# Performance work log

Hardware: AMD Instinct MI355X
Metric: run time of the kernel (lower is better)

Reference implementation:

```python
import jax, jax.numpy as jnp
import numpy as np
import math

D = 1024      # d_model
H = 4096      # expert hidden
E = 8         # num_experts
K = 2         # top_k
CAP_FACTOR = 1.25
B, S = 4, 2048
T = B * S
CAP = int(math.ceil(CAP_FACTOR * T * K / E))  # 2560


def setup_inputs() -> dict:
    key = jax.random.key(0)
    ks = jax.random.split(key, 6)
    x  = jax.random.normal(ks[0], (B, S, D), dtype=jnp.float32)
    Wr = jax.random.normal(ks[1], (D, E), dtype=jnp.float32) * (1.0 / np.sqrt(D))
    W1 = jax.random.normal(ks[2], (E, D, H), dtype=jnp.float32) * (1.0 / np.sqrt(D))
    b1 = jnp.zeros((E, H), dtype=jnp.float32)
    W2 = jax.random.normal(ks[3], (E, H, D), dtype=jnp.float32) * (1.0 / np.sqrt(H))
    b2 = jnp.zeros((E, D), dtype=jnp.float32)
    return {"x": x, "Wr": Wr, "W1": W1, "b1": b1, "W2": W2, "b2": b2}


def reference(x, Wr, W1, b1, W2, b2):
    x_flat = x.reshape(T, D)

    # ---- Router: top-k softmax gating (temp = 1.0), renormalized weights ----
    logits = jnp.einsum('td,de->te', x_flat, Wr)
    probs = jax.nn.softmax(logits, axis=-1)
    topk_w, topk_idx = jax.lax.top_k(probs, K)            # [T,K]
    topk_w = topk_w / jnp.sum(topk_w, axis=-1, keepdims=True)

    # ---- Vectorized capacity-based dispatch ----
    e = topk_idx.reshape(-1)                               # [T*K] expert id per pair
    onehot = jax.nn.one_hot(e, E, dtype=jnp.int32)         # [T*K, E]
    pos_all = jnp.cumsum(onehot, axis=0) - 1               # slot within expert
    pos = jnp.take_along_axis(pos_all, e[:, None], axis=1)[:, 0]
    keep = pos < CAP
    # dropped pairs go to a dummy slot E*CAP (sliced off / zero-padded)
    dest = jnp.where(keep, e * CAP + pos, E * CAP)         # [T*K]

    x_pairs = jnp.repeat(x_flat, K, axis=0)                # [T*K, D]
    buf = jnp.zeros((E * CAP + 1, D), dtype=x.dtype).at[dest].set(x_pairs)
    expert_in = buf[:E * CAP].reshape(E, CAP, D)

    # ---- Grouped expert MLP (GELU) ----
    h = jax.nn.gelu(jnp.einsum('ecd,edh->ech', expert_in, W1) + b1[:, None, :])
    expert_out = jnp.einsum('ech,ehd->ecd', h, W2) + b2[:, None, :]

    # ---- Combine: gather back and weight; dropped tokens get zeros ----
    out_pad = jnp.concatenate(
        [expert_out.reshape(E * CAP, D), jnp.zeros((1, D), dtype=x.dtype)], axis=0)
    y_pairs = out_pad[dest] * topk_w.reshape(-1)[:, None]  # [T*K, D]
    y_flat = y_pairs.reshape(T, K, D).sum(axis=1)
    return y_flat.reshape(B, S, D)
```

## Files before the change

### kernel.cpp

```cpp
#include <hip/hip_runtime.h>
#include <stdint.h>

#define D_MODEL 1024
#define H_DIM   4096
#define NE      8
#define NCAP    2560
#define NTOK    8192
#define NPAIR   (NTOK * 2)

typedef __attribute__((ext_vector_type(8))) __bf16 bf16x8;
typedef __attribute__((ext_vector_type(4))) float  f32x4;
typedef __attribute__((ext_vector_type(8))) unsigned short ushort8;

__device__ __forceinline__ unsigned short f2bf(float f) {
  union { float f; unsigned u; } v; v.f = f;
  unsigned r = v.u + 0x7fffu + ((v.u >> 16) & 1u);
  return (unsigned short)(r >> 16);
}
__device__ __forceinline__ float bf2f(unsigned short s) {
  union { unsigned u; float f; } v; v.u = ((unsigned)s) << 16;
  return v.f;
}
__device__ __forceinline__ float gelu_tanh(float x) {
  float u = 0.7978845608028654f * (x + 0.044715f * x * x * x);
  float e = __expf(2.0f * u);
  float th = 1.0f - 2.0f / (e + 1.0f);
  return 0.5f * x * (1.0f + th);
}
__device__ __forceinline__ void load_lds16(const void* g, void* l) {
  __builtin_amdgcn_global_load_lds(
      (const __attribute__((address_space(1))) unsigned int*)g,
      (__attribute__((address_space(3))) unsigned int*)l, 16, 0, 0);
}

__global__ __launch_bounds__(256) void router_kernel(
    const float* __restrict__ x, const float* __restrict__ Wr,
    int* __restrict__ pair_e, float* __restrict__ pair_w) {
  int lane = threadIdx.x & 63;
  int t = blockIdx.x * 4 + (threadIdx.x >> 6);
  float acc[NE];
#pragma unroll
  for (int e = 0; e < NE; ++e) acc[e] = 0.0f;
  const float* xr = x + (size_t)t * D_MODEL;
  for (int d = lane; d < D_MODEL; d += 64) {
    float xv = xr[d];
#pragma unroll
    for (int e = 0; e < NE; ++e) acc[e] = fmaf(xv, Wr[d * NE + e], acc[e]);
  }
#pragma unroll
  for (int off = 32; off > 0; off >>= 1) {
#pragma unroll
    for (int e = 0; e < NE; ++e) acc[e] += __shfl_down(acc[e], off, 64);
  }
  if (lane == 0) {
    int i1 = 0;
#pragma unroll
    for (int e = 1; e < NE; ++e) if (acc[e] > acc[i1]) i1 = e;
    int i2 = (i1 == 0) ? 1 : 0;
#pragma unroll
    for (int e = 0; e < NE; ++e) if (e != i1 && acc[e] > acc[i2]) i2 = e;
    float p2 = expf(acc[i2] - acc[i1]);
    float inv = 1.0f / (1.0f + p2);
    pair_e[t * 2]     = i1;  pair_e[t * 2 + 1] = i2;
    pair_w[t * 2]     = inv;
    pair_w[t * 2 + 1] = p2 * inv;
  }
}

__global__ __launch_bounds__(1024) void assign_kernel(
    const int* __restrict__ pair_e, int* __restrict__ pair_dest,
    int* __restrict__ counts) {
  __shared__ int wtot[16][NE];
  const int tid = threadIdx.x;
  const int lane = tid & 63, w = tid >> 6;

  int ids[16];
  const int4* pe = (const int4*)(pair_e + tid * 16);
#pragma unroll
  for (int q = 0; q < 4; ++q) {
    int4 v = pe[q];
    ids[q * 4 + 0] = v.x; ids[q * 4 + 1] = v.y;
    ids[q * 4 + 2] = v.z; ids[q * 4 + 3] = v.w;
  }
  int c[NE];
#pragma unroll
  for (int e = 0; e < NE; ++e) c[e] = 0;
#pragma unroll
  for (int j = 0; j < 16; ++j) c[ids[j]]++;

  int incl[NE];
#pragma unroll
  for (int e = 0; e < NE; ++e) incl[e] = c[e];
#pragma unroll
  for (int d = 1; d < 64; d <<= 1) {
#pragma unroll
    for (int e = 0; e < NE; ++e) {
      int u = __shfl_up(incl[e], d, 64);
      if (lane >= d) incl[e] += u;
    }
  }
  if (lane == 63) {
#pragma unroll
    for (int e = 0; e < NE; ++e) wtot[w][e] = incl[e];
  }
  __syncthreads();
  if (tid < NE) {
    int run = 0;
#pragma unroll
    for (int ww = 0; ww < 16; ++ww) {
      int t2 = wtot[ww][tid];
      wtot[ww][tid] = run;
      run += t2;
    }
    counts[tid] = run < NCAP ? run : NCAP;
  }
  __syncthreads();

  int off[NE];
#pragma unroll
  for (int e = 0; e < NE; ++e) off[e] = wtot[w][e] + incl[e] - c[e];
#pragma unroll
  for (int j = 0; j < 16; ++j) {
    int e = ids[j];
    int pos = off[e]++;
    pair_dest[tid * 16 + j] = (pos < NCAP) ? (e * NCAP + pos) : (NE * NCAP);
  }
}

__global__ __launch_bounds__(64) void dispatch_kernel(
    const float* __restrict__ x, const int* __restrict__ pair_dest,
    unsigned short* __restrict__ Xd) {
  int i = blockIdx.x;
  int dest = pair_dest[i];
  if (dest >= NE * NCAP) return;
  int lane = threadIdx.x;
  int t = i >> 1;
  const float4* xr = (const float4*)(x + (size_t)t * D_MODEL);
  ushort4* dr = (ushort4*)(Xd + (size_t)dest * D_MODEL);
#pragma unroll
  for (int c = 0; c < 4; ++c) {
    float4 v = xr[lane + c * 64];
    ushort4 o;
    o.x = f2bf(v.x); o.y = f2bf(v.y); o.z = f2bf(v.z); o.w = f2bf(v.w);
    dr[lane + c * 64] = o;
  }
}

__global__ __launch_bounds__(256) void transpose_cvt(
    const float* __restrict__ src, unsigned short* __restrict__ dst,
    int R, int C) {
  __shared__ float tile[64][69];
  int e = blockIdx.z;
  int c0 = blockIdx.x * 64, r0 = blockIdx.y * 64;
  const float* s = src + (size_t)e * R * C + (size_t)r0 * C + c0;
  int tc = (threadIdx.x & 15) * 4;
  int tr = threadIdx.x >> 4;
#pragma unroll
  for (int it = 0; it < 4; ++it) {
    int row = tr + it * 16;
    float4 v = *(const float4*)(s + (size_t)row * C + tc);
    tile[row][tc]     = v.x; tile[row][tc + 1] = v.y;
    tile[row][tc + 2] = v.z; tile[row][tc + 3] = v.w;
  }
  __syncthreads();
  unsigned short* d = dst + (size_t)e * R * C + (size_t)c0 * R + r0;
  int oc  = threadIdx.x >> 3;
  int orr = (threadIdx.x & 7) * 8;
#pragma unroll
  for (int it = 0; it < 2; ++it) {
    int crow = oc + it * 32;
    ushort8 v;
#pragma unroll
    for (int j = 0; j < 8; ++j) v[j] = f2bf(tile[orr + j][crow]);
    *(ushort8*)(d + (size_t)crow * R + orr) = v;
  }
}

__global__ __launch_bounds__(512, 2) void moe_gemm_pipe(
    const unsigned short* __restrict__ Abase,
    const unsigned short* __restrict__ Bbase,
    const float* __restrict__ bias,
    unsigned short* __restrict__ Cout,
    const int* __restrict__ counts,
    int N, int K, int NX, int do_gelu) {
  const int M = NCAP;
  const int KT = K >> 5;
  __shared__ char smem[131072];

  int orig = blockIdx.x;
  int q = (NX * NE) >> 3;
  int wgid = (orig & 7) * q + (orig >> 3);
  const int e = wgid / NX;
  int r = wgid % NX;

  int grp = r >> 2, lid = r & 3;
  int gm = grp % 5, gn = grp / 5;
  const int m0 = (gm * 2 + (lid & 1)) * 256;
  const int n0 = (gn * 2 + (lid >> 1)) * 256;
  if (m0 >= counts[e]) return;

  const int tid = threadIdx.x;
  const int lane = tid & 63;
  const int wid = tid >> 6;
  const int wm = (wid >> 2) * 128;
  const int wn = (wid & 3) * 64;

  const unsigned short* A = Abase + (size_t)e * M * K;
  const unsigned short* B = Bbase + (size_t)e * N * K;

  f32x4 acc[8][4];
  f32x4 zero = {0.f, 0.f, 0.f, 0.f};
#pragma unroll
  for (int i = 0; i < 8; ++i)
#pragma unroll
    for (int j = 0; j < 4; ++j) acc[i][j] = zero;

  const unsigned short* ga[2];
  const unsigned short* gb[2];
  int ldsoA[2], ldsoB[2];
#pragma unroll
  for (int c = 0; c < 2; ++c) {
    int ci = c * 512 + tid;
    int row = ci >> 2;
    int gch = (ci & 3) ^ ((row >> 1) & 3);
    ga[c] = A + (size_t)(m0 + row) * K + gch * 8;
    gb[c] = B + (size_t)(n0 + row) * K + gch * 8;
    ldsoA[c] = (c * 512 + wid * 64) * 16;
    ldsoB[c] = 16384 + (c * 512 + wid * 64) * 16;
  }

#define STAGE_TILE(slot)                                        \
  {                                                             \
    char* Sb = smem + (slot) * 32768;                           \
    _Pragma("unroll")                                           \
    for (int c = 0; c < 2; ++c) {                               \
      load_lds16(ga[c], Sb + ldsoA[c]);  ga[c] += 32;           \
      load_lds16(gb[c], Sb + ldsoB[c]);  gb[c] += 32;           \
    }                                                           \
  }

  STAGE_TILE(0)
  STAGE_TILE(1)
  STAGE_TILE(2)

  for (int kt = 0; kt < KT; ++kt) {
    int rem = KT - 1 - kt;
    if (rem >= 2)      { asm volatile("s_waitcnt vmcnt(8)" ::: "memory"); }
    else if (rem == 1) { asm volatile("s_waitcnt vmcnt(4)" ::: "memory"); }
    else               { asm volatile("s_waitcnt vmcnt(0)" ::: "memory"); }
    __builtin_amdgcn_sched_barrier(0);
    __builtin_amdgcn_s_barrier();
    __builtin_amdgcn_sched_barrier(0);

    if (kt + 3 < KT) STAGE_TILE((kt + 3) & 3)

    const char* Ab = smem + (size_t)(kt & 3) * 32768;
    const char* Bb = Ab + 16384;
    bf16x8 af[8], bfr[4];
    int lc = lane >> 4;
#pragma unroll
    for (int f = 0; f < 8; ++f) {
      int ar = wm + f * 16 + (lane & 15);
      af[f] = *(const bf16x8*)(Ab + ar * 64 + ((lc ^ ((ar >> 1) & 3)) * 16));
    }
#pragma unroll
    for (int f = 0; f < 4; ++f) {
      int br = wn + f * 16 + (lane & 15);
      bfr[f] = *(const bf16x8*)(Bb + br * 64 + ((lc ^ ((br >> 1) & 3)) * 16));
    }
    __builtin_amdgcn_s_setprio(1);
#pragma unroll
    for (int i = 0; i < 8; ++i)
#pragma unroll
      for (int j = 0; j < 4; ++j)
        acc[i][j] = __builtin_amdgcn_mfma_f32_16x16x32_bf16(
            af[i], bfr[j], acc[i][j], 0, 0, 0);
    __builtin_amdgcn_s_setprio(0);
  }
#undef STAGE_TILE

  __syncthreads();
  const float* be = bias + (size_t)e * N;
#pragma unroll
  for (int i = 0; i < 8; ++i) {
    int rbase = wm + i * 16 + ((lane >> 4) << 2);
#pragma unroll
    for (int j = 0; j < 4; ++j) {
      int col = wn + j * 16 + (lane & 15);
      float bv = be[n0 + col];
#pragma unroll
      for (int r2 = 0; r2 < 4; ++r2) {
        float xv = acc[i][j][r2] + bv;
        if (do_gelu) xv = gelu_tanh(xv);
        *(unsigned short*)(smem + (size_t)(rbase + r2) * 512 + col * 2) = f2bf(xv);
      }
    }
  }
  __syncthreads();
#pragma unroll
  for (int it = 0; it < 16; ++it) {
    int idx = it * 4096 + tid * 8;
    int row = idx >> 8, col = idx & 255;
    ushort8 v = *(const ushort8*)(smem + (size_t)idx * 2);
    *(ushort8*)(Cout + ((size_t)e * M + m0 + row) * N + n0 + col) = v;
  }
}

__global__ __launch_bounds__(256) void combine_kernel(
    const unsigned short* __restrict__ Ebuf,
    const int* __restrict__ pair_dest,
    const float* __restrict__ pair_w,
    float* __restrict__ out) {
  int t = blockIdx.x;
  int d0 = threadIdx.x * 4;
  float4 r = {0.f, 0.f, 0.f, 0.f};
#pragma unroll
  for (int k = 0; k < 2; ++k) {
    int dest = pair_dest[t * 2 + k];
    if (dest < NE * NCAP) {
      float w = pair_w[t * 2 + k];
      ushort4 v = *(const ushort4*)(Ebuf + (size_t)dest * D_MODEL + d0);
      r.x += w * bf2f(v.x); r.y += w * bf2f(v.y);
      r.z += w * bf2f(v.z); r.w += w * bf2f(v.w);
    }
  }
  *(float4*)(out + (size_t)t * D_MODEL + d0) = r;
}

extern "C" void kernel_launch(void* const* d_in, const int* in_sizes, int n_in,
                              void* d_out, int out_size, void* d_ws, size_t ws_size,
                              hipStream_t stream) {
  const float* x  = (const float*)d_in[0];
  const float* Wr = (const float*)d_in[1];
  const float* W1 = (const float*)d_in[2];
  const float* b1 = (const float*)d_in[3];
  const float* W2 = (const float*)d_in[4];
  const float* b2 = (const float*)d_in[5];
  float* out = (float*)d_out;

  char* ws = (char*)d_ws;
  unsigned short* W1T  = (unsigned short*)(ws + 0);
  unsigned short* W2T  = (unsigned short*)(ws + 67108864);
  unsigned short* Xd   = (unsigned short*)(ws + 134217728);
  unsigned short* Ebuf = Xd;
  unsigned short* Hbuf = (unsigned short*)(ws + 176160768);
  int*   pair_e    = (int*)(ws + 343932928);
  float* pair_w    = (float*)(ws + 343998464);
  int*   pair_dest = (int*)(ws + 344064000);
  int*   counts    = (int*)(ws + 344129536);

  transpose_cvt<<<dim3(H_DIM / 64, D_MODEL / 64, NE), 256, 0, stream>>>(W1, W1T, D_MODEL, H_DIM);
  transpose_cvt<<<dim3(D_MODEL / 64, H_DIM / 64, NE), 256, 0, stream>>>(W2, W2T, H_DIM, D_MODEL);

  router_kernel<<<NTOK / 4, 256, 0, stream>>>(x, Wr, pair_e, pair_w);
  assign_kernel<<<1, 1024, 0, stream>>>(pair_e, pair_dest, counts);
  dispatch_kernel<<<NPAIR, 64, 0, stream>>>(x, pair_dest, Xd);

  {
    int nx = (NCAP / 256) * (H_DIM / 256);
    moe_gemm_pipe<<<nx * NE, 512, 0, stream>>>(
        Xd, W1T, b1, Hbuf, counts, H_DIM, D_MODEL, nx, 1);
  }
  {
    int nx = (NCAP / 256) * (D_MODEL / 256);
    moe_gemm_pipe<<<nx * NE, 512, 0, stream>>>(
        Hbuf, W2T, b2, Ebuf, counts, D_MODEL, H_DIM, nx, 0);
  }

  combine_kernel<<<NTOK, 256, 0, stream>>>(Ebuf, pair_dest, pair_w, out);
}
```

Before: 819.5 us.

## Restructure expert GEMM main loop into 64-wide K tiles with interleaved staging

The GEMM main loop switches from a 4-deep ring of 32-wide K tiles to a double-buffered layout of 64-wide K tiles, processed two at a time. Each tile is split into four phases (two K halves by two M halves), with global-to-LDS loads for the next tile issued between MFMA clusters and barriers separating the phases. The goal is finer-grained overlap of memory loads, LDS reads and MFMA work, with fewer fragment registers live at once. The cost is more barriers and tighter vmcnt bookkeeping, and the per-wave row mapping in the epilogue changes to match the new M-half split.

```diff
diff --git a/kernel.cpp b/kernel.cpp
--- a/kernel.cpp
+++ b/kernel.cpp
@@ -184,7 +184,7 @@
     const int* __restrict__ counts,
     int N, int K, int NX, int do_gelu) {
   const int M = NCAP;
-  const int KT = K >> 5;
+  const int KT2 = K >> 7;
   __shared__ char smem[131072];
 
   int orig = blockIdx.x;
@@ -215,75 +215,110 @@
 #pragma unroll
     for (int j = 0; j < 4; ++j) acc[i][j] = zero;
 
-  const unsigned short* ga[2];
-  const unsigned short* gb[2];
-  int ldsoA[2], ldsoB[2];
-#pragma unroll
-  for (int c = 0; c < 2; ++c) {
-    int ci = c * 512 + tid;
-    int row = ci >> 2;
-    int gch = (ci & 3) ^ ((row >> 1) & 3);
-    ga[c] = A + (size_t)(m0 + row) * K + gch * 8;
-    gb[c] = B + (size_t)(n0 + row) * K + gch * 8;
-    ldsoA[c] = (c * 512 + wid * 64) * 16;
-    ldsoB[c] = 16384 + (c * 512 + wid * 64) * 16;
-  }
-
-#define STAGE_TILE(slot)                                        \
-  {                                                             \
-    char* Sb = smem + (slot) * 32768;                           \
-    _Pragma("unroll")                                           \
-    for (int c = 0; c < 2; ++c) {                               \
-      load_lds16(ga[c], Sb + ldsoA[c]);  ga[c] += 32;           \
-      load_lds16(gb[c], Sb + ldsoB[c]);  gb[c] += 32;           \
-    }                                                           \
-  }
-
-  STAGE_TILE(0)
-  STAGE_TILE(1)
-  STAGE_TILE(2)
-
-  for (int kt = 0; kt < KT; ++kt) {
-    int rem = KT - 1 - kt;
-    if (rem >= 2)      { asm volatile("s_waitcnt vmcnt(8)" ::: "memory"); }
-    else if (rem == 1) { asm volatile("s_waitcnt vmcnt(4)" ::: "memory"); }
-    else               { asm volatile("s_waitcnt vmcnt(0)" ::: "memory"); }
-    __builtin_amdgcn_sched_barrier(0);
-    __builtin_amdgcn_s_barrier();
-    __builtin_amdgcn_sched_barrier(0);
-
-    if (kt + 3 < KT) STAGE_TILE((kt + 3) & 3)
-
-    const char* Ab = smem + (size_t)(kt & 3) * 32768;
-    const char* Bb = Ab + 16384;
-    bf16x8 af[8], bfr[4];
-    int lc = lane >> 4;
-#pragma unroll
-    for (int f = 0; f < 8; ++f) {
-      int ar = wm + f * 16 + (lane & 15);
-      af[f] = *(const bf16x8*)(Ab + ar * 64 + ((lc ^ ((ar >> 1) & 3)) * 16));
+  const size_t soA = (size_t)(m0 + (tid >> 3)) * K + ((tid & 7) ^ ((tid >> 3) & 7)) * 8;
+  const size_t soB = (size_t)(n0 + (tid >> 3)) * K + ((tid & 7) ^ ((tid >> 3) & 7)) * 8;
+  const int wdst = wid * 1024;
+
+  const int sw0 = (((lane >> 4) + 0) ^ (lane & 7)) * 16;
+  const int sw1 = (((lane >> 4) + 4) ^ (lane & 7)) * 16;
+  const int abase = wm + (lane & 15);
+  const int bbase = wn + (lane & 15);
+
+#define STAGE_A(tile, half) do {                                           \
+    char* _d = smem + ((tile) & 1) * 65536 + (half) * 8192 + wdst;         \
+    const unsigned short* _s = A + soA + (size_t)(half) * 64 * K + (tile) * 64; \
+    load_lds16(_s, _d);                                                    \
+    load_lds16(_s + (size_t)128 * K, _d + 16384);                          \
+  } while (0)
+#define STAGE_B(tile, half) do {                                           \
+    char* _d = smem + ((tile) & 1) * 65536 + 32768 + (half) * 16384 + wdst; \
+    const unsigned short* _s = B + soB + (size_t)(half) * 128 * K + (tile) * 64; \
+    load_lds16(_s, _d);                                                    \
+    load_lds16(_s + (size_t)64 * K, _d + 8192);                            \
+  } while (0)
+
+#define DS_READS(tile, kk, mh) do {                                        \
+    const char* _Ab = smem + ((tile) & 1) * 65536;                         \
+    const char* _Bb = _Ab + 32768;                                         \
+    _Pragma("unroll")                                                      \
+    for (int f = 0; f < 4; ++f)                                            \
+      af[f] = *(const bf16x8*)(_Ab + (abase + (mh) * 64 + f * 16) * 128 + sw##kk); \
+    if ((mh) == 0) {                                                       \
+      _Pragma("unroll")                                                    \
+      for (int f = 0; f < 4; ++f)                                          \
+        bfr[f] = *(const bf16x8*)(_Bb + (bbase + f * 16) * 128 + sw##kk);  \
+    }                                                                      \
+  } while (0)
+
+#define MFMA_CLUSTER(mh) do {                                              \
+    asm volatile("s_waitcnt lgkmcnt(0)" ::: "memory");                     \
+    __builtin_amdgcn_sched_barrier(0);                                     \
+    __builtin_amdgcn_s_setprio(1);                                        \
+    _Pragma("unroll")                                                      \
+    for (int i = 0; i < 4; ++i)                                            \
+      _Pragma("unroll")                                                    \
+      for (int j = 0; j < 4; ++j)                                          \
+        acc[(mh) * 4 + i][j] = __builtin_amdgcn_mfma_f32_16x16x32_bf16(    \
+            af[i], bfr[j], acc[(mh) * 4 + i][j], 0, 0, 0);                 \
+    __builtin_amdgcn_s_setprio(0);                                        \
+    __builtin_amdgcn_s_barrier();                                          \
+  } while (0)
+
+#define PHASE_BODY(tile, kk, mh) do {                                      \
+    DS_READS(tile, kk, mh);                                                \
+    __builtin_amdgcn_sched_barrier(0);                                     \
+    __builtin_amdgcn_s_barrier();                                          \
+    MFMA_CLUSTER(mh);                                                      \
+  } while (0)
+
+#define PHASE_FIRST(tile, kk, mh) do {                                     \
+    __builtin_amdgcn_sched_barrier(0);                                     \
+    __builtin_amdgcn_s_barrier();                                          \
+    __builtin_amdgcn_sched_barrier(0);                                     \
+    DS_READS(tile, kk, mh);                                                \
+    MFMA_CLUSTER(mh);                                                      \
+  } while (0)
+
+  STAGE_A(0, 0); STAGE_A(0, 1); STAGE_B(0, 0); STAGE_B(0, 1); STAGE_A(1, 0);
+
+  for (int it = 0; it < KT2; ++it) {
+    const int t0 = 2 * it, t1 = 2 * it + 1;
+    const bool notlast = (it < KT2 - 1);
+    bf16x8 af[4], bfr[4];
+    STAGE_A(t1, 1);
+    asm volatile("s_waitcnt vmcnt(4)" ::: "memory");
+    PHASE_FIRST(t0, 0, 0);
+    STAGE_B(t1, 0);
+    PHASE_BODY(t0, 0, 1);
+    STAGE_B(t1, 1);
+    PHASE_BODY(t0, 1, 0);
+    if (notlast) STAGE_A(t0 + 2, 0);
+    PHASE_BODY(t0, 1, 1);
+    if (notlast) {
+      STAGE_A(t0 + 2, 1);
+      asm volatile("s_waitcnt vmcnt(4)" ::: "memory");
+    } else {
+      asm volatile("s_waitcnt vmcnt(0)" ::: "memory");
     }
-#pragma unroll
-    for (int f = 0; f < 4; ++f) {
-      int br = wn + f * 16 + (lane & 15);
-      bfr[f] = *(const bf16x8*)(Bb + br * 64 + ((lc ^ ((br >> 1) & 3)) * 16));
-    }
-    __builtin_amdgcn_s_setprio(1);
-#pragma unroll
-    for (int i = 0; i < 8; ++i)
-#pragma unroll
-      for (int j = 0; j < 4; ++j)
-        acc[i][j] = __builtin_amdgcn_mfma_f32_16x16x32_bf16(
-            af[i], bfr[j], acc[i][j], 0, 0, 0);
-    __builtin_amdgcn_s_setprio(0);
-  }
-#undef STAGE_TILE
-
-  __syncthreads();
+    PHASE_FIRST(t1, 0, 0);
+    if (notlast) STAGE_B(t0 + 2, 0);
+    PHASE_BODY(t1, 0, 1);
+    if (notlast) STAGE_B(t0 + 2, 1);
+    PHASE_BODY(t1, 1, 0);
+    if (notlast) STAGE_A(t1 + 2, 0);
+    PHASE_BODY(t1, 1, 1);
+  }
+#undef STAGE_A
+#undef STAGE_B
+#undef DS_READS
+#undef MFMA_CLUSTER
+#undef PHASE_BODY
+#undef PHASE_FIRST
+
   const float* be = bias + (size_t)e * N;
 #pragma unroll
   for (int i = 0; i < 8; ++i) {
-    int rbase = wm + i * 16 + ((lane >> 4) << 2);
+    int rbase = wm + (i & 3) * 16 + (i >> 2) * 64 + ((lane >> 4) << 2);
 #pragma unroll
     for (int j = 0; j < 4; ++j) {
       int col = wn + j * 16 + (lane & 15);
```

Result: slower. 847.8 us (+3.5%).
